# Performance work log

Hardware: AMD Instinct MI355X
Metric: run time of the kernel (lower is better)

Reference implementation:

```python
import jax, jax.numpy as jnp
import numpy as np

# E2M1 (FP4) representable magnitudes and rounding midpoints
LEVELS = jnp.array([0.0, 0.5, 1.0, 1.5, 2.0, 3.0, 4.0, 6.0], dtype=jnp.float32)
BOUNDS = jnp.array([0.25, 0.75, 1.25, 1.75, 2.5, 3.5, 5.0], dtype=jnp.float32)
E2M1_MAX = 6.0
EPS = 1e-12


def e2m1_block_quant_dequant(x, block_size):
    """Block-wise E2M1 fake-quantization along the last dim.

    Per block of `block_size` elements: scale = absmax / 6.0, then
    round-to-nearest onto the E2M1 grid {0,.5,1,1.5,2,3,4,6} (signed)
    and dequantize. Returns (dequantized x, per-block scales).
    """
    shape = x.shape
    nb = shape[-1] // block_size
    xb = x.reshape(*shape[:-1], nb, block_size)
    amax = jnp.max(jnp.abs(xb), axis=-1, keepdims=True)          # [..., nb, 1]
    scale = jnp.maximum(amax / E2M1_MAX, EPS)
    v = xb / scale
    mag = jnp.abs(v)
    # nearest E2M1 level: count how many rounding boundaries |v| exceeds
    idx = jnp.sum((mag[..., None] > BOUNDS).astype(jnp.int32), axis=-1)
    q = jnp.sign(v) * LEVELS[idx] * scale                        # dequantized
    return q.reshape(shape), scale[..., 0]


def setup_inputs() -> dict:
    key = jax.random.key(0)
    k1, k2, k3 = jax.random.split(key, 3)
    x = jax.random.normal(k1, (8, 1500, 1280), dtype=jnp.float32)
    weight = jax.random.normal(k2, (5120, 1280), dtype=jnp.float32) * 0.02
    bias = jax.random.normal(k3, (5120,), dtype=jnp.float32) * 0.01
    return {"x": x, "weight": weight, "bias": bias}


def reference(x, weight, bias):
    # activation quant (block_size_act = 32, along feature dim)
    x_q, _ = e2m1_block_quant_dequant(x, 32)
    # weight quant (block_size_w = 32, along in_features dim)
    w_q, scale_w = e2m1_block_quant_dequant(weight, 32)
    # F.linear: x @ W^T + b
    out = jnp.einsum('bsi,oi->bso', x_q, w_q) + bias
    return (out, scale_w)
```

## Files before the change

kernel.cpp:

```cpp
#include <hip/hip_runtime.h>
#include <hip/hip_fp16.h>


typedef _Float16 f16;
typedef _Float16 f16x8 __attribute__((ext_vector_type(8)));
typedef float f32x4 __attribute__((ext_vector_type(4)));

#define M_ROWS 12000
#define M_PAD  12032
#define N_COLS 5120
#define K_DIM  1280
#define KB     40
#define NTN    20

#define BAR()   asm volatile("s_barrier" ::: "memory")
#define VMCNT(N) asm volatile("s_waitcnt vmcnt(%0)" :: "i"(N) : "memory")
#define GLDS(gp, lp) __builtin_amdgcn_global_load_lds( \
    (const __attribute__((address_space(1))) unsigned*)(gp), \
    (__attribute__((address_space(3))) unsigned*)(lp), 16, 0, 0)

__device__ __forceinline__ float e2m1_level(float a) {
    float lv;
    if (a > 2.5f)       lv = (a > 3.5f) ? ((a > 5.0f) ? 6.0f : 4.0f) : 3.0f;
    else if (a > 1.25f) lv = (a > 1.75f) ? 2.0f : 1.5f;
    else                lv = (a > 0.75f) ? 1.0f : ((a > 0.25f) ? 0.5f : 0.0f);
    return lv;
}

__global__ __launch_bounds__(256) void quant_x_kernel(const float* __restrict__ x,
                                                      f16* __restrict__ xq) {
    int t = blockIdx.x * blockDim.x + threadIdx.x;
    int row = t / 160;
    int c8  = t % 160;
    f16x8 o;
    if (row < M_ROWS) {
        const float* p = x + (size_t)row * K_DIM + c8 * 8;
        float v[8];
        *(float4*)&v[0] = *(const float4*)p;
        *(float4*)&v[4] = *(const float4*)(p + 4);
        float am = 0.0f;
        #pragma unroll
        for (int i = 0; i < 8; ++i) am = fmaxf(am, fabsf(v[i]));
        am = fmaxf(am, __shfl_xor(am, 1));
        am = fmaxf(am, __shfl_xor(am, 2));
        float scale = fmaxf(am / 6.0f, 1e-12f);
        #pragma unroll
        for (int i = 0; i < 8; ++i) {
            float tq = v[i] / scale;
            float q  = copysignf(e2m1_level(fabsf(tq)), tq) * scale;
            o[i] = (f16)q;
        }
    } else {
        #pragma unroll
        for (int i = 0; i < 8; ++i) o[i] = (f16)0.0f;
    }
    *(f16x8*)(xq + (size_t)row * K_DIM + c8 * 8) = o;
}

__global__ __launch_bounds__(256) void quant_w_kernel(const float* __restrict__ w,
                                                      f16* __restrict__ wq,
                                                      float* __restrict__ scale_out) {
    int t = blockIdx.x * blockDim.x + threadIdx.x;
    int row = t / 160;
    int c8  = t % 160;
    const float* p = w + (size_t)row * K_DIM + c8 * 8;
    float v[8];
    *(float4*)&v[0] = *(const float4*)p;
    *(float4*)&v[4] = *(const float4*)(p + 4);
    float am = 0.0f;
    #pragma unroll
    for (int i = 0; i < 8; ++i) am = fmaxf(am, fabsf(v[i]));
    am = fmaxf(am, __shfl_xor(am, 1));
    am = fmaxf(am, __shfl_xor(am, 2));
    float scale = fmaxf(am / 6.0f, 1e-12f);
    if ((t & 3) == 0) scale_out[row * KB + (c8 >> 2)] = scale;
    f16x8 o;
    #pragma unroll
    for (int i = 0; i < 8; ++i) {
        float tq = v[i] / scale;
        float q  = copysignf(e2m1_level(fabsf(tq)), tq) * scale;
        o[i] = (f16)q;
    }
    *(f16x8*)(wq + (size_t)row * K_DIM + c8 * 8) = o;
}


__device__ __forceinline__ void stage_half(const f16* __restrict__ g, f16* l, int tid) {
    #pragma unroll
    for (int s = 0; s < 2; ++s) {
        int j = s * 512 + tid;
        int r = j >> 3;
        int c = (j & 7) ^ (r & 7);
        GLDS(g + (size_t)r * K_DIM + c * 8, l + (size_t)j * 8);
    }
}

#define READ_A(dst, buf, rbase)                                              \
    _Pragma("unroll")                                                        \
    for (int fm = 0; fm < 4; ++fm) {                                         \
        dst[fm][0] = *(const f16x8*)&(buf)[((rbase) + fm * 16) * 64 + swz[0]]; \
        dst[fm][1] = *(const f16x8*)&(buf)[((rbase) + fm * 16) * 64 + swz[1]]; \
    }
#define READ_B(dst, buf, rbase)                                              \
    _Pragma("unroll")                                                        \
    for (int fn = 0; fn < 2; ++fn) {                                         \
        dst[fn][0] = *(const f16x8*)&(buf)[((rbase) + fn * 16) * 64 + swz[0]]; \
        dst[fn][1] = *(const f16x8*)&(buf)[((rbase) + fn * 16) * 64 + swz[1]]; \
    }
#define MFMA_Q(ma, mb, mo, no)                                               \
    __builtin_amdgcn_s_setprio(1);                                           \
    _Pragma("unroll")                                                        \
    for (int fm = 0; fm < 4; ++fm)                                           \
        _Pragma("unroll")                                                    \
        for (int fn = 0; fn < 2; ++fn) {                                     \
            acc[fm + mo][fn + no] = __builtin_amdgcn_mfma_f32_16x16x32_f16(  \
                ma[fm][0], mb[fn][0], acc[fm + mo][fn + no], 0, 0, 0);       \
            acc[fm + mo][fn + no] = __builtin_amdgcn_mfma_f32_16x16x32_f16(  \
                ma[fm][1], mb[fn][1], acc[fm + mo][fn + no], 0, 0, 0);       \
        }                                                                    \
    __builtin_amdgcn_s_setprio(0);

template<bool SREST, int V4>
__device__ __forceinline__ void iter8(f16* A0, f16* B0, f16* A1, f16* B1,
                                      const f16* gA1, const f16* gA2,
                                      const f16* gB2, const f16* gB3,
                                      f32x4 (&acc)[8][4],
                                      int tid, int arow0, int brow0, const int (&swz)[2]) {
    f16x8 aLO[4][2], aHI[4][2], bLO[2][2], bHI[2][2];

    stage_half(gA1, A1, tid);
    READ_A(aLO, A0, arow0);
    READ_B(bLO, B0, brow0);
    MFMA_Q(aLO, bLO, 0, 0);
    BAR();
    stage_half(gA1 + 128 * K_DIM, A1 + 8192, tid);
    READ_B(bHI, B0, brow0 + 32);
    MFMA_Q(aLO, bHI, 0, 2);
    BAR();
    if (SREST) stage_half(gB2, B0, tid);
    READ_A(aHI, A0, arow0 + 64);
    MFMA_Q(aHI, bHI, 4, 2);
    BAR();
    if (SREST) stage_half(gA2, A0, tid);
    MFMA_Q(aHI, bLO, 4, 0);
    VMCNT(V4);
    BAR();
    if (SREST) stage_half(gA2 + 128 * K_DIM, A0 + 8192, tid);
    READ_A(aLO, A1, arow0);
    READ_B(bLO, B1, brow0);
    MFMA_Q(aLO, bLO, 0, 0);
    BAR();
    if (SREST) stage_half(gB2 + 128 * K_DIM, B0 + 8192, tid);
    READ_B(bHI, B1, brow0 + 32);
    MFMA_Q(aLO, bHI, 0, 2);
    BAR();
    if (SREST) stage_half(gB3, B1, tid);
    READ_A(aHI, A1, arow0 + 64);
    MFMA_Q(aHI, bHI, 4, 2);
    BAR();
    if (SREST) stage_half(gB3 + 128 * K_DIM, B1 + 8192, tid);
    MFMA_Q(aHI, bLO, 4, 0);
    if (SREST) VMCNT(4);
    BAR();
}

__global__ __launch_bounds__(512, 2) void gemm_kernel(const f16* __restrict__ A,
                                                      const f16* __restrict__ B,
                                                      const float* __restrict__ bias,
                                                      float* __restrict__ C) {
    extern __shared__ f16 sm[];
    int mt = blockIdx.x / NTN;
    int nt = blockIdx.x % NTN;

    int tid  = threadIdx.x;
    int lane = tid & 63;
    int wid  = tid >> 6;
    int wr   = wid >> 2;
    int wc   = wid & 3;
    int l15  = lane & 15;

    int swz[2] = { (((lane >> 4)    ) ^ (lane & 7)) * 8,
                   (((lane >> 4) + 4) ^ (lane & 7)) * 8 };
    int arow0 = wr * 128 + l15;
    int brow0 = wc * 64 + l15;

    const f16* gAb = A + (size_t)(mt * 256) * K_DIM;
    const f16* gBb = B + (size_t)(nt * 256) * K_DIM;

    f16* A0 = sm;
    f16* B0 = sm + 16384;
    f16* A1 = sm + 32768;
    f16* B1 = sm + 49152;

    f32x4 acc[8][4] = {};

    stage_half(gBb,               B0,        tid);
    stage_half(gAb,               A0,        tid);
    stage_half(gAb + 128 * K_DIM, A0 + 8192, tid);
    stage_half(gBb + 128 * K_DIM, B0 + 8192, tid);
    stage_half(gBb + 64,               B1,        tid);
    stage_half(gBb + 64 + 128 * K_DIM, B1 + 8192, tid);
    VMCNT(4);
    BAR();

    for (int i = 0; i < 9; ++i) {
        const f16* gA1 = gAb + (2 * i + 1) * 64;
        const f16* gA2 = gAb + (2 * i + 2) * 64;
        const f16* gB2 = gBb + (2 * i + 2) * 64;
        const f16* gB3 = gBb + (2 * i + 3) * 64;
        iter8<true, 4>(A0, B0, A1, B1, gA1, gA2, gB2, gB3,
                       acc, tid, arow0, brow0, swz);
    }
    iter8<false, 0>(A0, B0, A1, B1, gAb + 19 * 64, gAb, gBb, gBb,
                    acc, tid, arow0, brow0, swz);

    int crow0 = mt * 256 + wr * 128;
    int ccol  = nt * 256 + wc * 64 + l15;
    float bz[4];
    #pragma unroll
    for (int fn = 0; fn < 4; ++fn) bz[fn] = bias[ccol + fn * 16];

    #pragma unroll
    for (int fm = 0; fm < 8; ++fm) {
        #pragma unroll
        for (int j = 0; j < 4; ++j) {
            int row = crow0 + fm * 16 + (lane >> 4) * 4 + j;
            if (row < M_ROWS) {
                float* cp = C + (size_t)row * N_COLS + ccol;
                #pragma unroll
                for (int fn = 0; fn < 4; ++fn)
                    cp[fn * 16] = acc[fm][fn][j] + bz[fn];
            }
        }
    }
}

extern "C" void kernel_launch(void* const* d_in, const int* in_sizes, int n_in,
                              void* d_out, int out_size, void* d_ws, size_t ws_size,
                              hipStream_t stream) {
    const float* x      = (const float*)d_in[0];
    const float* weight = (const float*)d_in[1];
    const float* bias   = (const float*)d_in[2];
    float* out     = (float*)d_out;
    float* scale_w = (float*)d_out + (size_t)M_ROWS * N_COLS;

    f16* xq = (f16*)d_ws;
    f16* wq = (f16*)((char*)d_ws + (size_t)M_PAD * K_DIM * sizeof(f16));

    (void)hipFuncSetAttribute((const void*)gemm_kernel,
                              hipFuncAttributeMaxDynamicSharedMemorySize, 131072);

    {
        int threads = M_PAD * (K_DIM / 8);
        quant_x_kernel<<<threads / 256, 256, 0, stream>>>(x, xq);
    }
    {
        int threads = N_COLS * (K_DIM / 8);
        quant_w_kernel<<<threads / 256, 256, 0, stream>>>(weight, wq, scale_w);
    }
    {
        int grid = (M_PAD / 256) * (N_COLS / 256);
        gemm_kernel<<<grid, 512, 131072, stream>>>(xq, wq, bias, out);
    }
}
```

Baseline: 195.2 us.

## Restructure GEMM main loop into per-k-tile pipeline with register prefetch of next tile

Result: slower. 233.5 us (+19.6%).

```diff
diff --git a/kernel.cpp b/kernel.cpp
--- a/kernel.cpp
+++ b/kernel.cpp
@@ -95,72 +95,57 @@
     }
 }
 
-#define READ_A(dst, buf, rbase)                                              \
-    _Pragma("unroll")                                                        \
-    for (int fm = 0; fm < 4; ++fm) {                                         \
+#define READ_A(dst, buf, rbase)                                                \
+    _Pragma("unroll")                                                          \
+    for (int fm = 0; fm < 4; ++fm) {                                           \
         dst[fm][0] = *(const f16x8*)&(buf)[((rbase) + fm * 16) * 64 + swz[0]]; \
         dst[fm][1] = *(const f16x8*)&(buf)[((rbase) + fm * 16) * 64 + swz[1]]; \
     }
-#define READ_B(dst, buf, rbase)                                              \
-    _Pragma("unroll")                                                        \
-    for (int fn = 0; fn < 2; ++fn) {                                         \
+#define READ_B(dst, buf, rbase)                                                \
+    _Pragma("unroll")                                                          \
+    for (int fn = 0; fn < 2; ++fn) {                                           \
         dst[fn][0] = *(const f16x8*)&(buf)[((rbase) + fn * 16) * 64 + swz[0]]; \
         dst[fn][1] = *(const f16x8*)&(buf)[((rbase) + fn * 16) * 64 + swz[1]]; \
     }
-#define MFMA_Q(ma, mb, mo, no)                                               \
-    __builtin_amdgcn_s_setprio(1);                                           \
-    _Pragma("unroll")                                                        \
-    for (int fm = 0; fm < 4; ++fm)                                           \
-        _Pragma("unroll")                                                    \
-        for (int fn = 0; fn < 2; ++fn) {                                     \
-            acc[fm + mo][fn + no] = __builtin_amdgcn_mfma_f32_16x16x32_f16(  \
-                ma[fm][0], mb[fn][0], acc[fm + mo][fn + no], 0, 0, 0);       \
-            acc[fm + mo][fn + no] = __builtin_amdgcn_mfma_f32_16x16x32_f16(  \
-                ma[fm][1], mb[fn][1], acc[fm + mo][fn + no], 0, 0, 0);       \
-        }                                                                    \
+#define MFMA_Q(ma, mb, mo, no)                                                 \
+    __builtin_amdgcn_s_setprio(1);                                             \
+    _Pragma("unroll")                                                          \
+    for (int fm = 0; fm < 4; ++fm)                                             \
+        _Pragma("unroll")                                                      \
+        for (int fn = 0; fn < 2; ++fn) {                                       \
+            acc[fm + mo][fn + no] = __builtin_amdgcn_mfma_f32_16x16x32_f16(    \
+                ma[fm][0], mb[fn][0], acc[fm + mo][fn + no], 0, 0, 0);         \
+            acc[fm + mo][fn + no] = __builtin_amdgcn_mfma_f32_16x16x32_f16(    \
+                ma[fm][1], mb[fn][1], acc[fm + mo][fn + no], 0, 0, 0);         \
+        }                                                                      \
     __builtin_amdgcn_s_setprio(0);
 
-template<bool SREST, int V4>
-__device__ __forceinline__ void iter8(f16* A0, f16* B0, f16* A1, f16* B1,
-                                      const f16* gA1, const f16* gA2,
-                                      const f16* gB2, const f16* gB3,
+template<int PAR, bool STAGE, bool VM, bool READNEXT>
+__device__ __forceinline__ void ktile(f16* Xa, f16* Xb,
+                                      const f16* Ya, const f16* Yb,
+                                      const f16* gA2, const f16* gB2,
+                                      f16x8 (&aLO)[4][2], f16x8 (&bLO)[2][2][2],
                                       f32x4 (&acc)[8][4],
                                       int tid, int arow0, int brow0, const int (&swz)[2]) {
-    f16x8 aLO[4][2], aHI[4][2], bLO[2][2], bHI[2][2];
-
-    stage_half(gA1, A1, tid);
-    READ_A(aLO, A0, arow0);
-    READ_B(bLO, B0, brow0);
-    MFMA_Q(aLO, bLO, 0, 0);
-    BAR();
-    stage_half(gA1 + 128 * K_DIM, A1 + 8192, tid);
-    READ_B(bHI, B0, brow0 + 32);
+    f16x8 bHI[2][2], aHI[4][2];
+
+    READ_B(bHI, Xb, brow0 + 32);
+    MFMA_Q(aLO, bLO[PAR], 0, 0);
+    BAR();
+
+    READ_A(aHI, Xa, arow0 + 64);
     MFMA_Q(aLO, bHI, 0, 2);
-    BAR();
-    if (SREST) stage_half(gB2, B0, tid);
-    READ_A(aHI, A0, arow0 + 64);
+    if (VM) VMCNT(0);
+    BAR();
+
+    if (STAGE) { stage_half(gB2, Xb, tid); stage_half(gB2 + 128 * K_DIM, Xb + 8192, tid); }
+    if (READNEXT) { READ_A(aLO, Ya, arow0); }
     MFMA_Q(aHI, bHI, 4, 2);
     BAR();
-    if (SREST) stage_half(gA2, A0, tid);
-    MFMA_Q(aHI, bLO, 4, 0);
-    VMCNT(V4);
-    BAR();
-    if (SREST) stage_half(gA2 + 128 * K_DIM, A0 + 8192, tid);
-    READ_A(aLO, A1, arow0);
-    READ_B(bLO, B1, brow0);
-    MFMA_Q(aLO, bLO, 0, 0);
-    BAR();
-    if (SREST) stage_half(gB2 + 128 * K_DIM, B0 + 8192, tid);
-    READ_B(bHI, B1, brow0 + 32);
-    MFMA_Q(aLO, bHI, 0, 2);
-    BAR();
-    if (SREST) stage_half(gB3, B1, tid);
-    READ_A(aHI, A1, arow0 + 64);
-    MFMA_Q(aHI, bHI, 4, 2);
-    BAR();
-    if (SREST) stage_half(gB3 + 128 * K_DIM, B1 + 8192, tid);
-    MFMA_Q(aHI, bLO, 4, 0);
-    if (SREST) VMCNT(4);
+
+    if (STAGE) { stage_half(gA2, Xa, tid); stage_half(gA2 + 128 * K_DIM, Xa + 8192, tid); }
+    if (READNEXT) { READ_B(bLO[1 - PAR], Yb, brow0); }
+    MFMA_Q(aHI, bLO[PAR], 4, 0);
     BAR();
 }
 
@@ -193,26 +178,35 @@
     f16* B1 = sm + 49152;
 
     f32x4 acc[8][4] = {};
-
-    stage_half(gBb,               B0,        tid);
+    f16x8 aLO[4][2];
+    f16x8 bLO[2][2][2];
+
     stage_half(gAb,               A0,        tid);
     stage_half(gAb + 128 * K_DIM, A0 + 8192, tid);
+    stage_half(gBb,               B0,        tid);
     stage_half(gBb + 128 * K_DIM, B0 + 8192, tid);
+    stage_half(gAb + 64,               A1,        tid);
+    stage_half(gAb + 64 + 128 * K_DIM, A1 + 8192, tid);
     stage_half(gBb + 64,               B1,        tid);
     stage_half(gBb + 64 + 128 * K_DIM, B1 + 8192, tid);
-    VMCNT(4);
-    BAR();
-
-    for (int i = 0; i < 9; ++i) {
-        const f16* gA1 = gAb + (2 * i + 1) * 64;
-        const f16* gA2 = gAb + (2 * i + 2) * 64;
-        const f16* gB2 = gBb + (2 * i + 2) * 64;
-        const f16* gB3 = gBb + (2 * i + 3) * 64;
-        iter8<true, 4>(A0, B0, A1, B1, gA1, gA2, gB2, gB3,
-                       acc, tid, arow0, brow0, swz);
-    }
-    iter8<false, 0>(A0, B0, A1, B1, gAb + 19 * 64, gAb, gBb, gBb,
-                    acc, tid, arow0, brow0, swz);
+    VMCNT(8);
+    BAR();
+    READ_A(aLO, A0, arow0);
+    READ_B(bLO[0], B0, brow0);
+
+    for (int tt = 0; tt < 9; ++tt) {
+        int t = 2 * tt;
+        ktile<0, true, true, true>(A0, B0, A1, B1,
+                                   gAb + (t + 2) * 64, gBb + (t + 2) * 64,
+                                   aLO, bLO, acc, tid, arow0, brow0, swz);
+        ktile<1, true, true, true>(A1, B1, A0, B0,
+                                   gAb + (t + 3) * 64, gBb + (t + 3) * 64,
+                                   aLO, bLO, acc, tid, arow0, brow0, swz);
+    }
+    ktile<0, false, true, true>(A0, B0, A1, B1, gAb, gBb,
+                                aLO, bLO, acc, tid, arow0, brow0, swz);
+    ktile<1, false, false, false>(A1, B1, A0, B0, gAb, gBb,
+                                  aLO, bLO, acc, tid, arow0, brow0, swz);
 
     int crow0 = mt * 256 + wr * 128;
     int ccol  = nt * 256 + wc * 64 + l15;
```
